# Kernel tuning notes

Hardware: AMD Instinct MI355X
Metric: run time of the kernel (lower is better)

The kernel has to match this reference:

```python
import jax, jax.numpy as jnp
import numpy as np
from functools import partial

EPS = 1e-12  # F.normalize eps (clamp_min on the norm)


def conv2d(x, w, b, groups=1):
    # x: [B, Cin, H, W], w: [Cout, Cin//groups, 3, 3], 'same' padding, stride 1
    y = jax.lax.conv_general_dilated(
        x, w, window_strides=(1, 1), padding='SAME',
        dimension_numbers=('NCHW', 'OIHW', 'NCHW'),
        feature_group_count=groups)
    return y + b[None, :, None, None]


def setup_inputs() -> dict:
    key = jax.random.key(0)
    ks = jax.random.split(key, 8)
    B, C, H, W = 16, 256, 32, 32
    HW = H * W
    T = 2  # tasks: seg, depth
    return {
        'features_seg': jax.random.normal(ks[0], (B, C, H, W), jnp.float32),
        'features_depth': jax.random.normal(ks[1], (B, C, H, W), jnp.float32),
        'proj_w_seg': jax.random.normal(ks[2], (C, C, 3, 3), jnp.float32) * 0.02,
        'proj_b_seg': jnp.zeros((C,), jnp.float32),
        'proj_w_depth': jax.random.normal(ks[3], (C, C, 3, 3), jnp.float32) * 0.02,
        'proj_b_depth': jnp.zeros((C,), jnp.float32),
        'fusion_w': jax.random.normal(ks[4], (HW, T, 3, 3), jnp.float32) * 0.02,
        'fusion_b': jnp.zeros((HW,), jnp.float32),
    }


def reference(features_seg, features_depth, proj_w_seg, proj_b_seg,
              proj_w_depth, proj_b_depth, fusion_w, fusion_b):
    gamma = 0.5
    feats = [features_seg, features_depth]
    proj = [(proj_w_seg, proj_b_seg), (proj_w_depth, proj_b_depth)]
    B, C, H, W = features_seg.shape
    HW = H * W

    # Per-task cosine-similarity affinity matrices [B, HW, HW]
    Ms = []
    for f in feats:
        fv = f.reshape(B, C, HW)
        fn = fv / jnp.maximum(jnp.linalg.norm(fv, axis=1, keepdims=True), EPS)
        aff = jnp.einsum('bci,bcj->bij', fn, fn)  # [B, HW, HW]
        Ms.append(aff.reshape(B, HW, H, W))

    # Stack on dim=2 then flatten -> interleaved channels [B, HW*T, H, W]
    M = jnp.stack(Ms, axis=2).reshape(B, -1, H, W)
    M = conv2d(M, fusion_w, fusion_b, groups=HW)  # [B, HW, H, W]

    attention = M.reshape(B, HW, HW).transpose(0, 2, 1)  # [B, HW, HW]

    outs = []
    for f, (w, b) in zip(feats, proj):
        value = conv2d(f, w, b).reshape(B, C, HW)          # [B, C, HW]
        attended = jnp.einsum('bck,bkj->bcj', value, attention)
        attended = attended.reshape(B, C, H, W)
        outs.append(gamma * attended + (1.0 - gamma) * f)
    return tuple(outs)
```

## Files before the change

kernel.cpp:

```cpp
#include <hip/hip_runtime.h>
#include <hip/hip_bf16.h>

typedef __bf16 bf16;
typedef __attribute__((ext_vector_type(8))) __bf16 bf16x8;
typedef __attribute__((ext_vector_type(4))) __bf16 bf16x4v;
typedef __attribute__((ext_vector_type(4))) float f32x4;

#define B_  16
#define C_  256
#define HW_ 1024
#define PADR 1156
#define ZSTR 295936
#define TP  133

__device__ __forceinline__ void gll16(const bf16* g, bf16* l) {
  __builtin_amdgcn_global_load_lds((const __attribute__((address_space(1))) void*)g,
                                   (__attribute__((address_space(3))) void*)l, 16, 0, 0);
}

__global__ void prep_fat(const float* __restrict__ f0, const float* __restrict__ f1,
                         const float* __restrict__ w0, const float* __restrict__ w1,
                         bf16* __restrict__ fTpad, float* __restrict__ rn,
                         bf16* __restrict__ Wr) {
  int tid = threadIdx.x;
  if (blockIdx.x >= 1024) {
    int i = (blockIdx.x - 1024) * 256 + tid;
    int t = i / 589824, r2 = i % 589824;
    int c = r2 / 2304, r = r2 % 2304;
    int cin = r / 9, d = r % 9;
    Wr[(size_t)t * 589824 + c * 2304 + d * 256 + cin] = (bf16)(t ? w1 : w0)[r2];
    return;
  }
  __shared__ float sm[256][33];
  __shared__ float ps[8][32];
  int bx = blockIdx.x & 31, z = blockIdx.x >> 5;
  int t = z >> 4, b = z & 15;
  int k0 = bx * 32;
  const float* fb = (t ? f1 : f0) + (size_t)b * C_ * HW_ + k0;
  int kk = tid & 31, cg = tid >> 5;
  float ssq = 0.f;
  #pragma unroll
  for (int i = 0; i < 32; ++i) {
    int c = cg + i * 8;
    float v = fb[(size_t)c * HW_ + kk];
    sm[c][kk] = v;
    ssq += v * v;
  }
  ps[cg][kk] = ssq;

  bf16x8 zv;
  #pragma unroll
  for (int e = 0; e < 8; ++e) zv[e] = (bf16)0.f;
  if (tid < 64) {
    int c = (tid & 31) * 8, side = tid >> 5;
    *(bf16x8*)(fTpad + ((size_t)z * PADR + (bx + 1) * 34 + side * 33) * C_ + c) = zv;
  }
  if (bx == 0 || bx == 31) {
    int prow = (bx == 0) ? 0 : 33;
    for (int q = tid; q < 34 * 32; q += 256) {
      int wcol = q >> 5, c = (q & 31) * 8;
      *(bf16x8*)(fTpad + ((size_t)z * PADR + prow * 34 + wcol) * C_ + c) = zv;
    }
  }

  __syncthreads();
  if (tid < 32) {
    float s = 0.f;
    #pragma unroll
    for (int r = 0; r < 8; ++r) s += ps[r][tid];
    rn[z * 1024 + k0 + tid] = 1.f / fmaxf(sqrtf(s), 1e-12f);
  }
  int wl = tid >> 3, c0 = (tid & 7) * 32;
  bf16* dst = fTpad + ((size_t)z * PADR + (bx + 1) * 34 + wl + 1) * C_ + c0;
  #pragma unroll
  for (int u = 0; u < 4; ++u) {
    bf16x8 vv;
    #pragma unroll
    for (int e = 0; e < 8; ++e) vv[e] = (bf16)sm[c0 + u * 8 + e][wl];
    *(bf16x8*)(dst + u * 8) = vv;
  }
}

__global__ void fusion_conv2(const bf16* __restrict__ aff, const float* __restrict__ fw,
                             const float* __restrict__ fb, bf16* __restrict__ M) {
  __shared__ float sa[2][1024];
  int bi = blockIdx.x;
  int i = bi & 1023, b = bi >> 10;
  int tid = threadIdx.x;
  #pragma unroll
  for (int t = 0; t < 2; ++t) {
    const bf16* arow = aff + (((size_t)t * 16 + b) * 1024 + i) * 1024;
    bf16x4v ch = ((const bf16x4v*)arow)[tid];
    sa[t][tid * 4 + 0] = (float)ch[0];
    sa[t][tid * 4 + 1] = (float)ch[1];
    sa[t][tid * 4 + 2] = (float)ch[2];
    sa[t][tid * 4 + 3] = (float)ch[3];
  }
  float wgt[2][9];
  #pragma unroll
  for (int t = 0; t < 2; ++t)
    #pragma unroll
    for (int q = 0; q < 9; ++q) wgt[t][q] = fw[i * 18 + t * 9 + q];
  float bias = fb[i];
  __syncthreads();
  #pragma unroll
  for (int s0 = 0; s0 < 4; ++s0) {
    int s = tid + s0 * 256;
    int h = s >> 5, w = s & 31;
    float acc = bias;
    #pragma unroll
    for (int kh = 0; kh < 3; ++kh) {
      int hh = h + kh - 1;
      if ((unsigned)hh < 32u) {
        #pragma unroll
        for (int kw = 0; kw < 3; ++kw) {
          int ww = w + kw - 1;
          if ((unsigned)ww < 32u) {
            acc += wgt[0][kh * 3 + kw] * sa[0][hh * 32 + ww];
            acc += wgt[1][kh * 3 + kw] * sa[1][hh * 32 + ww];
          }
        }
      }
    }
    M[((size_t)bi << 10) + s] = (bf16)acc;
  }
}

template<int MODE, int BM>
__device__ __forceinline__
void gemm_core(int bx, int by, int z, bf16* As, bf16* Bs, bf16* T,
               const bf16* __restrict__ A, long long sA,
               const bf16* __restrict__ Bm, long long sB, int K,
               bf16* __restrict__ Cb, long long sC,
               const float* __restrict__ x0, const float* __restrict__ x1,
               float* __restrict__ Co) {
  const int tt = (MODE == 1) ? (z >> 4) : (z & 1);
  const int bb = (MODE == 1) ? (z & 15) : (z >> 1);
  const int zold = tt * 16 + bb;
  const bf16* Ab = A + (size_t)z * sA;
  const bf16* Bb = Bm + (size_t)(MODE == 1 ? z : bb) * sB;
  const int m0 = by * BM, n0 = bx * 128;
  const int tid = threadIdx.x;
  const int lane = tid & 63, wave = tid >> 6;
  const int wm = (wave >> 1) * (BM / 2), wn = (wave & 1) * 64;
  const int fr = lane & 15, fq = lane >> 4;
  constexpr int MI = BM / 32;
  constexpr int SA = BM / 32;

  const bf16* srcA[SA];
  const bf16* srcB[4];
  int ldsA[SA], ldsB[4];
  #pragma unroll
  for (int s = 0; s < SA; ++s) {
    int q = (wave * SA + s) * 64 + lane;
    int row = q >> 3, c = (q & 7) ^ (row & 7);
    ldsA[s] = __builtin_amdgcn_readfirstlane((wave * SA + s) * 512);
    if (MODE == 1) {
      int j = m0 + row;
      srcA[s] = Ab + (size_t)(((j >> 5) + 1) * 34 + (j & 31) + 1) * C_ + c * 8;
    } else {
      srcA[s] = Ab + (size_t)(m0 + row) * K + c * 8;
    }
  }
  #pragma unroll
  for (int s = 0; s < 4; ++s) {
    int q = (wave * 4 + s) * 64 + lane;
    int row = q >> 3, c = (q & 7) ^ (row & 7);
    ldsB[s] = __builtin_amdgcn_readfirstlane((wave * 4 + s) * 512);
    int jb = n0 + row;
    if (MODE == 1) {
      srcB[s] = Bb + (size_t)(((jb >> 5) + 1) * 34 + (jb & 31) + 1) * C_ + c * 8;
    } else {
      srcB[s] = Bb + (size_t)jb * K + c * 8;
    }
  }
  int lA[2][MI], lB[2][4];
  #pragma unroll
  for (int h = 0; h < 2; ++h) {
    #pragma unroll
    for (int i = 0; i < MI; ++i) {
      int rr = wm + i * 16 + fr;
      lA[h][i] = rr * 64 + (((h * 4) + fq) ^ (rr & 7)) * 8;
    }
    #pragma unroll
    for (int j = 0; j < 4; ++j) {
      int rc = wn + j * 16 + fr;
      lB[h][j] = rc * 64 + (((h * 4) + fq) ^ (rc & 7)) * 8;
    }
  }

  f32x4 acc[MI][4];
  #pragma unroll
  for (int i = 0; i < MI; ++i)
    #pragma unroll
    for (int j = 0; j < 4; ++j) acc[i][j] = 0.f;

  for (int k0 = 0; k0 < K; k0 += 64) {
    #pragma unroll
    for (int s = 0; s < SA; ++s) gll16(srcA[s] + k0, As + ldsA[s]);
    #pragma unroll
    for (int s = 0; s < 4; ++s) gll16(srcB[s] + k0, Bs + ldsB[s]);
    __syncthreads();
    #pragma unroll
    for (int h = 0; h < 2; ++h) {
      bf16x8 af[MI], bfr[4];
      #pragma unroll
      for (int i = 0; i < MI; ++i) af[i] = *(const bf16x8*)(&As[lA[h][i]]);
      #pragma unroll
      for (int j = 0; j < 4; ++j) bfr[j] = *(const bf16x8*)(&Bs[lB[h][j]]);
      #pragma unroll
      for (int i = 0; i < MI; ++i)
        #pragma unroll
        for (int j = 0; j < 4; ++j)
          acc[i][j] = __builtin_amdgcn_mfma_f32_16x16x32_bf16(af[i], bfr[j], acc[i][j], 0, 0, 0);
    }
    __syncthreads();
  }

  const bool mirror = (MODE == 1) && (bx != by);
  #pragma unroll
  for (int i = 0; i < MI; ++i) {
    int rbase = m0 + wm + i * 16 + fq * 4;
    #pragma unroll
    for (int j = 0; j < 4; ++j) {
      int col = n0 + wn + j * 16 + fr;
      float cj = (MODE == 1) ? x0[(size_t)z * 1024 + col] : 0.f;
      #pragma unroll
      for (int r = 0; r < 4; ++r) {
        int row = rbase + r;
        float v = acc[i][j][r];
        if (MODE == 1) {
          bf16 sv = (bf16)(v * x0[(size_t)z * 1024 + row] * cj);
          Cb[(size_t)z * sC + (size_t)row * 1024 + col] = sv;
          if (mirror) T[(row - m0) * TP + (col - n0)] = sv;
        } else {
          const float* fp = tt ? x1 : x0;
          Co[(size_t)zold * sC + (size_t)row * 1024 + col] =
              0.5f * v + 0.5f * fp[(size_t)bb * sC + (size_t)row * 1024 + col];
        }
      }
    }
  }
  if (mirror) {
    __syncthreads();
    #pragma unroll
    for (int s = 0; s < 8; ++s) {
      int q2 = s * 256 + tid;
      int g = q2 >> 4, c0 = (q2 & 15) << 3;
      bf16x8 vv;
      #pragma unroll
      for (int e = 0; e < 8; ++e) vv[e] = T[(c0 + e) * TP + g];
      *(bf16x8*)(Cb + (size_t)z * sC + (size_t)(n0 + g) * 1024 + m0 + c0) = vv;
    }
  }
}

__global__ __launch_bounds__(256, 4)
void gemm_aff(const bf16* __restrict__ fTpad, const float* __restrict__ rn,
              bf16* __restrict__ aff) {
  __shared__ bf16 smem[128 * TP];
  int q = blockIdx.x, by = 0, cnt = 8;
  while (q >= cnt) { q -= cnt; ++by; --cnt; }
  int bx = by + q;
  gemm_core<1, 128>(bx, by, blockIdx.z, smem, smem + 8192, smem,
                    fTpad, ZSTR, fTpad, ZSTR, C_,
                    aff, (long long)HW_ * HW_, rn, rn, nullptr);
}

__global__ __launch_bounds__(256, 4)
void gemm_attend(const bf16* __restrict__ value, const bf16* __restrict__ Mbuf,
                 const float* __restrict__ f0, const float* __restrict__ f1,
                 float* __restrict__ out) {
  __shared__ bf16 smem[128 * 128];
  gemm_core<2, 128>(blockIdx.x, blockIdx.y, blockIdx.z, smem, smem + 8192, smem,
                    value, (long long)C_ * HW_, Mbuf, (long long)HW_ * HW_, 1024,
                    nullptr, (long long)C_ * HW_, f0, f1, out);
}

__global__ __launch_bounds__(512, 2)
void gemm_value_p(const bf16* __restrict__ Wr, const bf16* __restrict__ fTpad,
                  bf16* __restrict__ value, const float* __restrict__ b0,
                  const float* __restrict__ b1) {
  __shared__ bf16 smem3[3 * 24576];
  const int z = blockIdx.y;
  const int tt = z & 1, bb = z >> 1, zold = tt * 16 + bb;
  const bf16* Ab = Wr + (size_t)tt * 589824;
  const bf16* Bb = fTpad + (size_t)zold * ZSTR;
  const int n0 = blockIdx.x * 128;
  const int tid = threadIdx.x;
  const int lane = tid & 63, wave = tid >> 6;
  const int wm = (wave >> 1) * 64, wn = (wave & 1) * 64;
  const int fr = lane & 15, fq = lane >> 4;

  const bf16* srcA[4]; int ldsA[4];
  #pragma unroll
  for (int s = 0; s < 4; ++s) {
    int q = s * 512 + tid;
    int row = q >> 3, c = (q & 7) ^ (row & 7);
    ldsA[s] = __builtin_amdgcn_readfirstlane(s * 4096 + wave * 512);
    srcA[s] = Ab + (size_t)row * 2304 + c * 8;
  }
  const bf16* srcB[2]; int ldsB[2];
  #pragma unroll
  for (int s = 0; s < 2; ++s) {
    int q = s * 512 + tid;
    int row = q >> 3, c = (q & 7) ^ (row & 7);
    ldsB[s] = __builtin_amdgcn_readfirstlane(s * 4096 + wave * 512);
    int jb = n0 + row;
    srcB[s] = Bb + (size_t)(((jb >> 5) + 1) * 34 + (jb & 31) + 1) * C_ + c * 8;
  }

  int lA[2][4], lB[2][4];
  #pragma unroll
  for (int h = 0; h < 2; ++h) {
    #pragma unroll
    for (int i = 0; i < 4; ++i) {
      int rr = wm + i * 16 + fr;
      lA[h][i] = rr * 64 + (((h * 4) + fq) ^ (rr & 7)) * 8;
      int rc = wn + i * 16 + fr;
      lB[h][i] = rc * 64 + (((h * 4) + fq) ^ (rc & 7)) * 8;
    }
  }

  auto STAGE = [&](int t, int bufi) {
    int k0 = t * 64;
    int d = k0 >> 8;
    int kh = d / 3, kw = d - kh * 3;
    int boff = ((kh - 1) * 34 + (kw - 1)) * C_ + (k0 & 255);
    bf16* As = smem3 + bufi * 24576;
    bf16* Bs = As + 16384;
    #pragma unroll
    for (int s = 0; s < 4; ++s) gll16(srcA[s] + k0, As + ldsA[s]);
    #pragma unroll
    for (int s = 0; s < 2; ++s) gll16(srcB[s] + boff, Bs + ldsB[s]);
  };

  f32x4 acc[4][4];
  #pragma unroll
  for (int i = 0; i < 4; ++i)
    #pragma unroll
    for (int j = 0; j < 4; ++j) acc[i][j] = 0.f;

  STAGE(0, 0);
  STAGE(1, 1);

  int cur = 0;
  #pragma unroll 1
  for (int t = 0; t < 36; ++t) {
    if (t < 35) asm volatile("s_waitcnt vmcnt(6)" ::: "memory");
    else        asm volatile("s_waitcnt vmcnt(0)" ::: "memory");
    __builtin_amdgcn_s_barrier();
    asm volatile("" ::: "memory");
    if (t + 2 < 36) {
      int nx = cur + 2; if (nx >= 3) nx -= 3;
      STAGE(t + 2, nx);
    }
    bf16* As = smem3 + cur * 24576;
    bf16* Bs = As + 16384;
    #pragma unroll
    for (int h = 0; h < 2; ++h) {
      bf16x8 af[4], bv[4];
      #pragma unroll
      for (int i = 0; i < 4; ++i) af[i] = *(const bf16x8*)(As + lA[h][i]);
      #pragma unroll
      for (int j = 0; j < 4; ++j) bv[j] = *(const bf16x8*)(Bs + lB[h][j]);
      __builtin_amdgcn_s_setprio(1);
      #pragma unroll
      for (int i = 0; i < 4; ++i)
        #pragma unroll
        for (int j = 0; j < 4; ++j)
          acc[i][j] = __builtin_amdgcn_mfma_f32_16x16x32_bf16(af[i], bv[j], acc[i][j], 0, 0, 0);
      __builtin_amdgcn_s_setprio(0);
    }
    ++cur; if (cur >= 3) cur = 0;
  }

  const float* bias = tt ? b1 : b0;
  #pragma unroll
  for (int i = 0; i < 4; ++i) {
    #pragma unroll
    for (int j = 0; j < 4; ++j) {
      int col = n0 + wn + j * 16 + fr;
      #pragma unroll
      for (int r = 0; r < 4; ++r) {
        int row = wm + i * 16 + fq * 4 + r;
        value[(size_t)z * ((size_t)C_ * HW_) + (size_t)row * 1024 + col] =
            (bf16)(acc[i][j][r] + bias[row]);
      }
    }
  }
}

extern "C" void kernel_launch(void* const* d_in, const int* in_sizes, int n_in,
                              void* d_out, int out_size, void* d_ws, size_t ws_size,
                              hipStream_t stream) {
  const float* f0 = (const float*)d_in[0];
  const float* f1 = (const float*)d_in[1];
  const float* w0 = (const float*)d_in[2];
  const float* b0 = (const float*)d_in[3];
  const float* w1 = (const float*)d_in[4];
  const float* b1 = (const float*)d_in[5];
  const float* fusion_w = (const float*)d_in[6];
  const float* fusion_b = (const float*)d_in[7];
  float* out = (float*)d_out;

  char* ws = (char*)d_ws;
  bf16* aff   = (bf16*)ws;
  bf16* Mbuf  = (bf16*)ws;
  bf16* fTpad = (bf16*)(ws + 67108864ull);
  bf16* Wr    = (bf16*)(ws + 86048768ull);
  bf16* value = (bf16*)(ws + 88408064ull);
  float* rn   = (float*)(ws + 105185280ull);

  prep_fat<<<5632, 256, 0, stream>>>(f0, f1, w0, w1, fTpad, rn, Wr);
  gemm_aff<<<dim3(36, 1, 32), 256, 0, stream>>>(fTpad, rn, aff);
  gemm_value_p<<<dim3(8, 32), 512, 0, stream>>>(Wr, fTpad, value, b0, b1);
  fusion_conv2<<<16384, 256, 0, stream>>>(aff, fusion_w, fusion_b, Mbuf);
  gemm_attend<<<dim3(8, 2, 32), 256, 0, stream>>>(value, Mbuf, f0, f1, out);
}
```

Measured before the change: 233.4 us.

## Load value-GEMM weights directly to registers and shrink LDS to B only

The conv-as-GEMM value kernel now loads its weight (A) fragments straight from global memory into registers, double-buffered one k-step ahead, instead of staging them through LDS. Only the activation (B) tiles still go through a triple-buffered LDS ring, which reduces LDS to a third of its former size. The k-loop is split into two half-steps with barriers and explicit waitcnts so the next B stage is issued mid-step. This removes LDS traffic and footprint for A, but adds register pressure, uncoalesced per-lane global loads of A that are served from cache across blocks, and more barriers per step.

```diff
diff --git a/kernel.cpp b/kernel.cpp
--- a/kernel.cpp
+++ b/kernel.cpp
@@ -277,11 +277,61 @@
                     nullptr, (long long)C_ * HW_, f0, f1, out);
 }
 
+#define VP_KSTEP(T_, ACUR, ANXT)                                               \
+  {                                                                            \
+    const int t_ = (T_);                                                       \
+    bf16* Bs_ = smem3 + (t_ % 3) * 8192;                                       \
+      \
+    {                                                                          \
+      bf16x8 bv[4];                                                            \
+      _Pragma("unroll")                                                        \
+      for (int j = 0; j < 4; ++j) bv[j] = *(const bf16x8*)(Bs_ + lB[0][j]);    \
+      if (t_ + 1 < 36) {                                                       \
+        _Pragma("unroll")                                                      \
+        for (int h = 0; h < 2; ++h)                                            \
+          _Pragma("unroll")                                                    \
+          for (int i = 0; i < 4; ++i)                                          \
+            ANXT[h][i] = *(const bf16x8*)(srcAr[i] + (t_ + 1) * 64 + h * 32);  \
+      }                                                                        \
+      asm volatile("s_waitcnt lgkmcnt(0)" ::: "memory");                       \
+      __builtin_amdgcn_sched_barrier(0);                                       \
+      __builtin_amdgcn_s_setprio(1);                                           \
+      _Pragma("unroll")                                                        \
+      for (int i = 0; i < 4; ++i)                                              \
+        _Pragma("unroll")                                                      \
+        for (int j = 0; j < 4; ++j)                                            \
+          acc[i][j] = __builtin_amdgcn_mfma_f32_16x16x32_bf16(                 \
+              ACUR[0][i], bv[j], acc[i][j], 0, 0, 0);                          \
+      __builtin_amdgcn_s_setprio(0);                                           \
+    }                                                                          \
+    __builtin_amdgcn_s_barrier();                                              \
+      \
+    {                                                                          \
+      bf16x8 bv[4];                                                            \
+      _Pragma("unroll")                                                        \
+      for (int j = 0; j < 4; ++j) bv[j] = *(const bf16x8*)(Bs_ + lB[1][j]);    \
+      if (t_ + 2 < 36) STAGE_B(t_ + 2, (t_ + 2) % 3);                          \
+      asm volatile("s_waitcnt lgkmcnt(0)" ::: "memory");                       \
+      __builtin_amdgcn_sched_barrier(0);                                       \
+      __builtin_amdgcn_s_setprio(1);                                           \
+      _Pragma("unroll")                                                        \
+      for (int i = 0; i < 4; ++i)                                              \
+        _Pragma("unroll")                                                      \
+        for (int j = 0; j < 4; ++j)                                            \
+          acc[i][j] = __builtin_amdgcn_mfma_f32_16x16x32_bf16(                 \
+              ACUR[1][i], bv[j], acc[i][j], 0, 0, 0);                          \
+      __builtin_amdgcn_s_setprio(0);                                           \
+      if (t_ < 34) asm volatile("s_waitcnt vmcnt(2)" ::: "memory");            \
+      else         asm volatile("s_waitcnt vmcnt(0)" ::: "memory");            \
+    }                                                                          \
+    __builtin_amdgcn_s_barrier();                                              \
+  }
+
 __global__ __launch_bounds__(512, 2)
 void gemm_value_p(const bf16* __restrict__ Wr, const bf16* __restrict__ fTpad,
                   bf16* __restrict__ value, const float* __restrict__ b0,
                   const float* __restrict__ b1) {
-  __shared__ bf16 smem3[3 * 24576];
+  __shared__ bf16 smem3[3 * 8192];
   const int z = blockIdx.y;
   const int tt = z & 1, bb = z >> 1, zold = tt * 16 + bb;
   const bf16* Ab = Wr + (size_t)tt * 589824;
@@ -292,14 +342,11 @@
   const int wm = (wave >> 1) * 64, wn = (wave & 1) * 64;
   const int fr = lane & 15, fq = lane >> 4;
 
-  const bf16* srcA[4]; int ldsA[4];
-  #pragma unroll
-  for (int s = 0; s < 4; ++s) {
-    int q = s * 512 + tid;
-    int row = q >> 3, c = (q & 7) ^ (row & 7);
-    ldsA[s] = __builtin_amdgcn_readfirstlane(s * 4096 + wave * 512);
-    srcA[s] = Ab + (size_t)row * 2304 + c * 8;
-  }
+  const bf16* srcAr[4];
+  #pragma unroll
+  for (int i = 0; i < 4; ++i)
+    srcAr[i] = Ab + (size_t)(wm + i * 16 + fr) * 2304 + fq * 8;
+
   const bf16* srcB[2]; int ldsB[2];
   #pragma unroll
   for (int s = 0; s < 2; ++s) {
@@ -310,29 +357,23 @@
     srcB[s] = Bb + (size_t)(((jb >> 5) + 1) * 34 + (jb & 31) + 1) * C_ + c * 8;
   }
 
-  int lA[2][4], lB[2][4];
-  #pragma unroll
-  for (int h = 0; h < 2; ++h) {
-    #pragma unroll
-    for (int i = 0; i < 4; ++i) {
-      int rr = wm + i * 16 + fr;
-      lA[h][i] = rr * 64 + (((h * 4) + fq) ^ (rr & 7)) * 8;
-      int rc = wn + i * 16 + fr;
-      lB[h][i] = rc * 64 + (((h * 4) + fq) ^ (rc & 7)) * 8;
-    }
-  }
-
-  auto STAGE = [&](int t, int bufi) {
+  int lB[2][4];
+  #pragma unroll
+  for (int h = 0; h < 2; ++h)
+    #pragma unroll
+    for (int j = 0; j < 4; ++j) {
+      int rc = wn + j * 16 + fr;
+      lB[h][j] = rc * 64 + (((h * 4) + fq) ^ (rc & 7)) * 8;
+    }
+
+  auto STAGE_B = [&](int t, int bufi) {
     int k0 = t * 64;
     int d = k0 >> 8;
     int kh = d / 3, kw = d - kh * 3;
     int boff = ((kh - 1) * 34 + (kw - 1)) * C_ + (k0 & 255);
-    bf16* As = smem3 + bufi * 24576;
-    bf16* Bs = As + 16384;
-    #pragma unroll
-    for (int s = 0; s < 4; ++s) gll16(srcA[s] + k0, As + ldsA[s]);
-    #pragma unroll
-    for (int s = 0; s < 2; ++s) gll16(srcB[s] + boff, Bs + ldsB[s]);
+    bf16* Bs = smem3 + bufi * 8192;
+    gll16(srcB[0] + boff, Bs + ldsB[0]);
+    gll16(srcB[1] + boff, Bs + ldsB[1]);
   };
 
   f32x4 acc[4][4];
@@ -341,38 +382,23 @@
     #pragma unroll
     for (int j = 0; j < 4; ++j) acc[i][j] = 0.f;
 
-  STAGE(0, 0);
-  STAGE(1, 1);
-
-  int cur = 0;
+  bf16x8 a0[2][4], a1[2][4];
+  #pragma unroll
+  for (int h = 0; h < 2; ++h)
+    #pragma unroll
+    for (int i = 0; i < 4; ++i)
+      a0[h][i] = *(const bf16x8*)(srcAr[i] + h * 32);
+  __builtin_amdgcn_sched_barrier(0);
+  STAGE_B(0, 0);
+  STAGE_B(1, 1);
+  __builtin_amdgcn_sched_barrier(0);
+  asm volatile("s_waitcnt vmcnt(2)" ::: "memory");
+  __builtin_amdgcn_s_barrier();
+
   #pragma unroll 1
-  for (int t = 0; t < 36; ++t) {
-    if (t < 35) asm volatile("s_waitcnt vmcnt(6)" ::: "memory");
-    else        asm volatile("s_waitcnt vmcnt(0)" ::: "memory");
-    __builtin_amdgcn_s_barrier();
-    asm volatile("" ::: "memory");
-    if (t + 2 < 36) {
-      int nx = cur + 2; if (nx >= 3) nx -= 3;
-      STAGE(t + 2, nx);
-    }
-    bf16* As = smem3 + cur * 24576;
-    bf16* Bs = As + 16384;
-    #pragma unroll
-    for (int h = 0; h < 2; ++h) {
-      bf16x8 af[4], bv[4];
-      #pragma unroll
-      for (int i = 0; i < 4; ++i) af[i] = *(const bf16x8*)(As + lA[h][i]);
-      #pragma unroll
-      for (int j = 0; j < 4; ++j) bv[j] = *(const bf16x8*)(Bs + lB[h][j]);
-      __builtin_amdgcn_s_setprio(1);
-      #pragma unroll
-      for (int i = 0; i < 4; ++i)
-        #pragma unroll
-        for (int j = 0; j < 4; ++j)
-          acc[i][j] = __builtin_amdgcn_mfma_f32_16x16x32_bf16(af[i], bv[j], acc[i][j], 0, 0, 0);
-      __builtin_amdgcn_s_setprio(0);
-    }
-    ++cur; if (cur >= 3) cur = 0;
+  for (int tp = 0; tp < 18; ++tp) {
+    VP_KSTEP(2 * tp,     a0, a1);
+    VP_KSTEP(2 * tp + 1, a1, a0);
   }
 
   const float* bias = tt ? b1 : b0;
```

After: 283.4 us. +21.4%, slower.
